# Performance work log

Hardware: AMD Instinct MI355X
Metric: run time of the kernel (lower is better)

Reference implementation:

```python
import jax, jax.numpy as jnp
import numpy as np

B, H, W, C = 16, 64, 64, 192
NH, WS, SHIFT = 6, 8, 4          # heads, window size, shift (window//2)
DEPTH, MLP_R = 2, 4
N = WS * WS                      # tokens per window = 64
HD = C // NH                     # head dim = 32
SCALE = HD ** -0.5
TBL = (2 * WS - 1) ** 2          # relative-bias table size = 225
NW = (H // WS) * (W // WS)       # windows per image = 64


def _rel_pos_index():
    coords = np.stack(np.meshgrid(np.arange(WS), np.arange(WS), indexing='ij')).reshape(2, -1)
    rel = (coords[:, :, None] - coords[:, None, :]).transpose(1, 2, 0)
    rel[..., 0] += WS - 1
    rel[..., 1] += WS - 1
    rel[..., 0] *= 2 * WS - 1
    return jnp.asarray(rel.sum(-1))  # [N, N] int


def _attn_mask():
    # Swin shifted-window mask: region ids then pairwise -100 where ids differ.
    img = np.zeros((H, W))
    sl = (slice(0, -WS), slice(-WS, -SHIFT), slice(-SHIFT, None))
    cnt = 0
    for hs in sl:
        for ws in sl:
            img[hs, ws] = cnt
            cnt += 1
    mw = img.reshape(H // WS, WS, W // WS, WS).transpose(0, 2, 1, 3).reshape(-1, N)
    diff = mw[:, None, :] - mw[:, :, None]
    return jnp.asarray(np.where(diff != 0, -100.0, 0.0).astype(np.float32))  # [NW, N, N]


REL_IDX = _rel_pos_index()
ATTN_MASK = _attn_mask()


def _ln(x, g, b, eps=1e-5):
    mu = x.mean(-1, keepdims=True)
    var = ((x - mu) ** 2).mean(-1, keepdims=True)
    return (x - mu) * jax.lax.rsqrt(var + eps) * g + b


def setup_inputs() -> dict:
    key = jax.random.key(0)
    ks = jax.random.split(key, 8)
    s = 0.02
    return {
        'x': jax.random.normal(ks[0], (B, H * W, C), jnp.float32),
        'norm1_g': jnp.ones((DEPTH, C)), 'norm1_b': jnp.zeros((DEPTH, C)),
        'qkv_w': jax.random.normal(ks[1], (DEPTH, 3 * C, C)) * s,
        'qkv_b': jnp.zeros((DEPTH, 3 * C)),
        'bias_table': jax.random.normal(ks[2], (DEPTH, TBL, NH)) * s,
        'proj_w': jax.random.normal(ks[3], (DEPTH, C, C)) * s,
        'proj_b': jnp.zeros((DEPTH, C)),
        'norm2_g': jnp.ones((DEPTH, C)), 'norm2_b': jnp.zeros((DEPTH, C)),
        'fc1_w': jax.random.normal(ks[4], (DEPTH, MLP_R * C, C)) * s,
        'fc1_b': jnp.zeros((DEPTH, MLP_R * C)),
        'fc2_w': jax.random.normal(ks[5], (DEPTH, C, MLP_R * C)) * s,
        'fc2_b': jnp.zeros((DEPTH, C)),
    }


def _block(x, shift, n1g, n1b, qw, qb, tbl, pw, pb, n2g, n2b, f1w, f1b, f2w, f2b):
    shortcut = x
    y = _ln(x, n1g, n1b).reshape(B, H, W, C)
    if shift > 0:
        y = jnp.roll(y, (-shift, -shift), axis=(1, 2))
    # window partition -> [B*NW, N, C]
    win = y.reshape(B, H // WS, WS, W // WS, WS, C).transpose(0, 1, 3, 2, 4, 5).reshape(-1, N, C)
    qkv = (win @ qw.T + qb).reshape(-1, N, 3, NH, HD).transpose(2, 0, 3, 1, 4)
    q, k, v = qkv[0] * SCALE, qkv[1], qkv[2]          # each [B*NW, NH, N, HD]
    attn = jnp.einsum('bhnd,bhmd->bhnm', q, k)
    attn = attn + tbl[REL_IDX].transpose(2, 0, 1)[None]  # relative position bias
    if shift > 0:
        attn = (attn.reshape(B, NW, NH, N, N) + ATTN_MASK[None, :, None]).reshape(-1, NH, N, N)
    attn = jax.nn.softmax(attn, axis=-1)
    o = jnp.einsum('bhnm,bhmd->bhnd', attn, v).transpose(0, 2, 1, 3).reshape(-1, N, C)
    o = o @ pw.T + pb
    # window reverse
    y = o.reshape(B, H // WS, W // WS, WS, WS, C).transpose(0, 1, 3, 2, 4, 5).reshape(B, H, W, C)
    if shift > 0:
        y = jnp.roll(y, (shift, shift), axis=(1, 2))
    x = shortcut + y.reshape(B, H * W, C)
    h = _ln(x, n2g, n2b)
    h = jax.nn.gelu(h @ f1w.T + f1b, approximate=False)  # torch nn.GELU = exact erf
    return x + (h @ f2w.T + f2b)


def reference(x, norm1_g, norm1_b, qkv_w, qkv_b, bias_table, proj_w, proj_b,
              norm2_g, norm2_b, fc1_w, fc1_b, fc2_w, fc2_b):
    for i in range(DEPTH):
        shift = 0 if i % 2 == 0 else SHIFT
        x = _block(x, shift, norm1_g[i], norm1_b[i], qkv_w[i], qkv_b[i], bias_table[i],
                   proj_w[i], proj_b[i], norm2_g[i], norm2_b[i],
                   fc1_w[i], fc1_b[i], fc2_w[i], fc2_b[i])
    return x
```

## Files before the change

### kernel.cpp

```cpp
#include <hip/hip_runtime.h>
#include <hip/hip_bf16.h>
#include <math.h>

typedef __hip_bfloat16 bf16;
typedef short bf16x8 __attribute__((ext_vector_type(8)));
typedef short s16x4 __attribute__((ext_vector_type(4)));
typedef float f32x4 __attribute__((ext_vector_type(4)));

#define TOKENS 65536
#define C_ 192

__device__ __forceinline__ float b2f(bf16 v){ return __bfloat162float(v); }
__device__ __forceinline__ bf16 f2b(float v){ return __float2bfloat16(v); }
__device__ __forceinline__ short f2s(float v){
  bf16 b = __float2bfloat16(v);
  union { bf16 b; short s; } u; u.b = b; return u.s;
}

__global__ void detect_k(const unsigned* __restrict__ g, int* __restrict__ flag){
  *flag = (g[0] == 0x3F800000u) ? 1 : 0;
}
__global__ void xconv_k(const void* __restrict__ x, float* __restrict__ y, int n,
                        const int* __restrict__ flag){
  int i = blockIdx.x*blockDim.x + threadIdx.x;
  if (i >= n) return;
  if (*flag) y[i] = ((const float*)x)[i];
  else       y[i] = b2f(((const bf16*)x)[i]);
}
struct WPtrs { const void* p[13]; };
__global__ void wconv_all_k(WPtrs wp, const int* __restrict__ offs, const int* __restrict__ lens,
                            bf16* __restrict__ dst, int total, const int* __restrict__ flag){
  int i = blockIdx.x*blockDim.x + threadIdx.x;
  if (i >= total) return;
  int t = 0;
  while (t < 12 && i >= offs[t+1]) t++;
  int j = i - offs[t];
  if (j >= lens[t]) return;
  if (*flag) dst[i] = f2b(((const float*)wp.p[t])[j]);
  else       dst[i] = ((const bf16*)wp.p[t])[j];
}
__global__ void outconv_k(const float* __restrict__ x, void* __restrict__ y, int n,
                          const int* __restrict__ flag){
  int i = blockIdx.x*blockDim.x + threadIdx.x;
  if (i >= n) return;
  if (*flag) ((float*)y)[i] = x[i];
  else       ((bf16*)y)[i]  = f2b(x[i]);
}

__global__ void bias_setup_k(const bf16* __restrict__ bt, float* __restrict__ biasF){
  int idx = blockIdx.x*blockDim.x + threadIdx.x;
  if (idx >= 2*6*64*64) return;
  int v = idx & 63;
  int lane = (idx >> 6) & 63;
  int rest = idx >> 12;
  int head = rest % 6, dd = rest / 6;
  int jt = v >> 4, it = (v >> 2) & 3, r = v & 3;
  int quad = lane >> 4, lr = lane & 15;
  int j = jt*16 + quad*4 + r;
  int i = it*16 + lr;
  int rel = ((i>>3) - (j>>3) + 7)*15 + ((i&7) - (j&7) + 7);
  biasF[idx] = b2f(bt[(dd*225 + rel)*6 + head]);
}

__global__ __launch_bounds__(384, 1) void attn_fused_k(float* __restrict__ xres,
    const bf16* __restrict__ n1g, const bf16* __restrict__ n1b,
    const bf16* __restrict__ qw, const bf16* __restrict__ qb,
    const bf16* __restrict__ pw, const bf16* __restrict__ pb,
    const float* __restrict__ biasF, int shift)
{
  extern __shared__ char smem[];
  short* xo = (short*)smem;
  int win = blockIdx.x;
  int tid = threadIdx.x;
  int wave = tid >> 6, lane = tid & 63;
  int quad = lane >> 4, lr = lane & 15;
  int b_ = win >> 6, wl = win & 63, wh = wl >> 3, wwi = wl & 7;
  short* kh  = (short*)(smem + 25600 + wave*17408);
  short* vth = kh + 2048;
  short* qP  = vth + 2304;

  int c0 = lane*3;
  float g0 = b2f(n1g[c0]), g1 = b2f(n1g[c0+1]), g2 = b2f(n1g[c0+2]);
  float e0 = b2f(n1b[c0]), e1 = b2f(n1b[c0+1]), e2 = b2f(n1b[c0+2]);
  for (int p = 0; p < 11; p++){
    int tok = p*6 + wave;
    if (tok < 64){
      int hh = (wh*8 + (tok>>3) + shift) & 63, ww = (wwi*8 + (tok&7) + shift) & 63;
      const float* rowp = xres + ((size_t)(b_<<12) + (hh<<6) + ww)*C_;
      float v0 = rowp[c0], v1 = rowp[c0+1], v2 = rowp[c0+2];
      float s = v0+v1+v2;
      #pragma unroll
      for (int off=32; off; off>>=1) s += __shfl_xor(s, off);
      float mu = s * (1.0f/192.0f);
      float d0=v0-mu, d1=v1-mu, d2=v2-mu;
      float q = d0*d0+d1*d1+d2*d2;
      #pragma unroll
      for (int off=32; off; off>>=1) q += __shfl_xor(q, off);
      float rstd = rsqrtf(q*(1.0f/192.0f) + 1e-5f);
      xo[tok*200 + c0]   = f2s(d0*rstd*g0 + e0);
      xo[tok*200 + c0+1] = f2s(d1*rstd*g1 + e1);
      xo[tok*200 + c0+2] = f2s(d2*rstd*g2 + e2);
    }
  }
  __syncthreads();

  int head = wave;
  const short* qwd = (const short*)qw;
  #pragma unroll
  for (int cc = 0; cc < 3; cc++){
    int nbase = cc*192 + head*32;
    f32x4 acc[2][4];
    #pragma unroll
    for (int mt = 0; mt < 2; mt++)
      #pragma unroll
      for (int nt = 0; nt < 4; nt++) acc[mt][nt] = (f32x4){0.f,0.f,0.f,0.f};
    #pragma unroll
    for (int ks = 0; ks < 6; ks++){
      bf16x8 af[2], bx[4];
      #pragma unroll
      for (int mt = 0; mt < 2; mt++)
        af[mt] = *(const bf16x8*)(qwd + (size_t)(nbase + mt*16 + lr)*192 + ks*32 + quad*8);
      #pragma unroll
      for (int nt = 0; nt < 4; nt++)
        bx[nt] = *(const bf16x8*)&xo[(nt*16 + lr)*200 + ks*32 + quad*8];
      #pragma unroll
      for (int mt = 0; mt < 2; mt++)
        #pragma unroll
        for (int nt = 0; nt < 4; nt++)
          acc[mt][nt] = __builtin_amdgcn_mfma_f32_16x16x32_bf16(af[mt], bx[nt], acc[mt][nt], 0, 0, 0);
    }
    #pragma unroll
    for (int mt = 0; mt < 2; mt++){
      float bv[4];
      #pragma unroll
      for (int r = 0; r < 4; r++) bv[r] = b2f(qb[nbase + mt*16 + quad*4 + r]);
      #pragma unroll
      for (int nt = 0; nt < 4; nt++){
        int tok = nt*16 + lr;
        if (cc == 0){
          s16x4 pk;
          #pragma unroll
          for (int r = 0; r < 4; r++) pk[r] = f2s((acc[mt][nt][r] + bv[r]) * 0.17677669529663689f);
          *(s16x4*)&qP[tok*32 + mt*16 + quad*4] = pk;
        } else if (cc == 1){
          s16x4 pk;
          #pragma unroll
          for (int r = 0; r < 4; r++) pk[r] = f2s(acc[mt][nt][r] + bv[r]);
          *(s16x4*)&kh[tok*32 + mt*16 + quad*4] = pk;
        } else {
          #pragma unroll
          for (int r = 0; r < 4; r++)
            vth[(mt*16 + quad*4 + r)*72 + tok] = f2s(acc[mt][nt][r] + bv[r]);
        }
      }
    }
  }
  __syncthreads();

  bf16x8 ak[4], bq[4];
  #pragma unroll
  for (int jt = 0; jt < 4; jt++) ak[jt] = *(const bf16x8*)&kh[(jt*16 + lr)*32 + quad*8];
  #pragma unroll
  for (int it = 0; it < 4; it++) bq[it] = *(const bf16x8*)&qP[(it*16 + lr)*32 + quad*8];

  f32x4 S[4][4];
  #pragma unroll
  for (int jt = 0; jt < 4; jt++)
    #pragma unroll
    for (int it = 0; it < 4; it++) S[jt][it] = (f32x4){0.f,0.f,0.f,0.f};
  #pragma unroll
  for (int jt = 0; jt < 4; jt++)
    #pragma unroll
    for (int it = 0; it < 4; it++)
      S[jt][it] = __builtin_amdgcn_mfma_f32_16x16x32_bf16(ak[jt], bq[it], S[jt][it], 0, 0, 0);

  const f32x4* bm = (const f32x4*)(biasF + ((size_t)head*64 + lane)*64);
  #pragma unroll
  for (int jt = 0; jt < 4; jt++)
    #pragma unroll
    for (int it = 0; it < 4; it++) S[jt][it] += bm[jt*4 + it];

  if (shift){
    int idi[4];
    #pragma unroll
    for (int it = 0; it < 4; it++){
      int hh = wh*8 + it*2 + (lr >> 3);
      int wwc = wwi*8 + (lr & 7);
      idi[it] = (hh < 56 ? 0 : (hh < 60 ? 1 : 2))*3 + (wwc < 56 ? 0 : (wwc < 60 ? 1 : 2));
    }
    #pragma unroll
    for (int jt = 0; jt < 4; jt++)
      #pragma unroll
      for (int r = 0; r < 4; r++){
        int j = jt*16 + quad*4 + r;
        int hh = wh*8 + (j >> 3), wwc = wwi*8 + (j & 7);
        int idj = (hh < 56 ? 0 : (hh < 60 ? 1 : 2))*3 + (wwc < 56 ? 0 : (wwc < 60 ? 1 : 2));
        #pragma unroll
        for (int it = 0; it < 4; it++)
          if (idj != idi[it]) S[jt][it][r] -= 100.f;
      }
  }
  #pragma unroll
  for (int it = 0; it < 4; it++){
    float m = -1e30f;
    #pragma unroll
    for (int jt = 0; jt < 4; jt++)
      #pragma unroll
      for (int r = 0; r < 4; r++) m = fmaxf(m, S[jt][it][r]);
    m = fmaxf(m, __shfl_xor(m, 16));
    m = fmaxf(m, __shfl_xor(m, 32));
    float s = 0.f;
    #pragma unroll
    for (int jt = 0; jt < 4; jt++)
      #pragma unroll
      for (int r = 0; r < 4; r++){
        float e = __expf(S[jt][it][r] - m);
        S[jt][it][r] = e; s += e;
      }
    s += __shfl_xor(s, 16);
    s += __shfl_xor(s, 32);
    float inv = 1.0f / s;
    #pragma unroll
    for (int jt = 0; jt < 4; jt++){
      s16x4 pk;
      #pragma unroll
      for (int r = 0; r < 4; r++) pk[r] = f2s(S[jt][it][r] * inv);
      *(s16x4*)&qP[(it*16 + lr)*68 + jt*16 + quad*4] = pk;
    }
  }

  bf16x8 va[2][2], pv[4][2];
  #pragma unroll
  for (int mt = 0; mt < 2; mt++)
    #pragma unroll
    for (int ks = 0; ks < 2; ks++)
      va[mt][ks] = *(const bf16x8*)&vth[(mt*16 + lr)*72 + ks*32 + quad*8];
  #pragma unroll
  for (int nt = 0; nt < 4; nt++)
    #pragma unroll
    for (int ks = 0; ks < 2; ks++)
      pv[nt][ks] = *(const bf16x8*)&qP[(nt*16 + lr)*68 + ks*32 + quad*8];

  f32x4 O[2][4];
  #pragma unroll
  for (int mt = 0; mt < 2; mt++)
    #pragma unroll
    for (int nt = 0; nt < 4; nt++) O[mt][nt] = (f32x4){0.f,0.f,0.f,0.f};
  #pragma unroll
  for (int mt = 0; mt < 2; mt++)
    #pragma unroll
    for (int nt = 0; nt < 4; nt++)
      #pragma unroll
      for (int ks = 0; ks < 2; ks++)
        O[mt][nt] = __builtin_amdgcn_mfma_f32_16x16x32_bf16(va[mt][ks], pv[nt][ks], O[mt][nt], 0, 0, 0);

  #pragma unroll
  for (int mt = 0; mt < 2; mt++)
    #pragma unroll
    for (int nt = 0; nt < 4; nt++){
      s16x4 pk;
      #pragma unroll
      for (int r = 0; r < 4; r++) pk[r] = f2s(O[mt][nt][r]);
      *(s16x4*)&xo[(nt*16 + lr)*200 + head*32 + mt*16 + quad*4] = pk;
    }
  __syncthreads();

  f32x4 po[4][2];
  #pragma unroll
  for (int mt = 0; mt < 4; mt++)
    #pragma unroll
    for (int nt = 0; nt < 2; nt++) po[mt][nt] = (f32x4){0.f,0.f,0.f,0.f};
  const short* pwd = (const short*)pw;
  #pragma unroll
  for (int ks = 0; ks < 6; ks++){
    bf16x8 ao[4], bw[2];
    #pragma unroll
    for (int mt = 0; mt < 4; mt++)
      ao[mt] = *(const bf16x8*)&xo[(mt*16 + lr)*200 + ks*32 + quad*8];
    #pragma unroll
    for (int nt = 0; nt < 2; nt++)
      bw[nt] = *(const bf16x8*)(pwd + (size_t)(head*32 + nt*16 + lr)*192 + ks*32 + quad*8);
    #pragma unroll
    for (int mt = 0; mt < 4; mt++)
      #pragma unroll
      for (int nt = 0; nt < 2; nt++)
        po[mt][nt] = __builtin_amdgcn_mfma_f32_16x16x32_bf16(ao[mt], bw[nt], po[mt][nt], 0, 0, 0);
  }
  #pragma unroll
  for (int nt = 0; nt < 2; nt++){
    int n = head*32 + nt*16 + lr;
    float bv = b2f(pb[n]);
    #pragma unroll
    for (int mt = 0; mt < 4; mt++){
      #pragma unroll
      for (int r = 0; r < 4; r++){
        int tok = mt*16 + quad*4 + r;
        int hh = (wh*8 + (tok>>3) + shift) & 63, ww = (wwi*8 + (tok&7) + shift) & 63;
        float* dst = xres + ((size_t)(b_<<12) + (hh<<6) + ww)*C_ + n;
        *dst += po[mt][nt][r] + bv;
      }
    }
  }
}

__global__ __launch_bounds__(384, 2) void mlp_fused_k(float* __restrict__ xres,
    const bf16* __restrict__ n2g, const bf16* __restrict__ n2b,
    const bf16* __restrict__ f1w, const bf16* __restrict__ f1b,
    const bf16* __restrict__ f2w, const bf16* __restrict__ f2bv)
{
  extern __shared__ char smem[];
  short* xh = (short*)smem;
  short* Hs = (short*)(smem + 51200);
  int t0 = blockIdx.x * 128;
  int tid = threadIdx.x;
  int wave = tid >> 6, lane = tid & 63;
  int quad = lane >> 4, lr = lane & 15;
  int wm = wave / 3, wn = wave % 3;

  int c0 = lane*3;
  float g0 = b2f(n2g[c0]), g1 = b2f(n2g[c0+1]), g2 = b2f(n2g[c0+2]);
  float e0 = b2f(n2b[c0]), e1 = b2f(n2b[c0+1]), e2 = b2f(n2b[c0+2]);
  for (int p = 0; p < 22; p++){
    int row = p*6 + wave;
    if (row < 128){
      const float* rowp = xres + (size_t)(t0 + row)*C_;
      float v0 = rowp[c0], v1 = rowp[c0+1], v2 = rowp[c0+2];
      float s = v0+v1+v2;
      #pragma unroll
      for (int off=32; off; off>>=1) s += __shfl_xor(s, off);
      float mu = s * (1.0f/192.0f);
      float d0=v0-mu, d1=v1-mu, d2=v2-mu;
      float q = d0*d0+d1*d1+d2*d2;
      #pragma unroll
      for (int off=32; off; off>>=1) q += __shfl_xor(q, off);
      float rstd = rsqrtf(q*(1.0f/192.0f) + 1e-5f);
      xh[row*200 + c0]   = f2s(d0*rstd*g0 + e0);
      xh[row*200 + c0+1] = f2s(d1*rstd*g1 + e1);
      xh[row*200 + c0+2] = f2s(d2*rstd*g2 + e2);
    }
  }
  __syncthreads();

  f32x4 acc2[4][4];
  #pragma unroll
  for (int i = 0; i < 4; i++)
    #pragma unroll
    for (int j = 0; j < 4; j++) acc2[i][j] = (f32x4){0.f,0.f,0.f,0.f};

  const short* f1 = (const short*)f1w;
  const short* f2 = (const short*)f2w;
  for (int cc = 0; cc < 8; cc++){
    int hb = cc*96;
    int h0 = hb + wave*16;
    f32x4 a1[8];
    #pragma unroll
    for (int nt = 0; nt < 8; nt++) a1[nt] = (f32x4){0.f,0.f,0.f,0.f};
    #pragma unroll
    for (int ks = 0; ks < 6; ks++){
      bf16x8 af = *(const bf16x8*)(f1 + (size_t)(h0 + lr)*192 + ks*32 + quad*8);
      #pragma unroll
      for (int nt = 0; nt < 8; nt++){
        bf16x8 bx = *(const bf16x8*)&xh[(nt*16 + lr)*200 + ks*32 + quad*8];
        a1[nt] = __builtin_amdgcn_mfma_f32_16x16x32_bf16(af, bx, a1[nt], 0, 0, 0);
      }
    }
    float bv1[4];
    #pragma unroll
    for (int r = 0; r < 4; r++) bv1[r] = b2f(f1b[h0 + quad*4 + r]);
    #pragma unroll
    for (int nt = 0; nt < 8; nt++){
      s16x4 pk;
      #pragma unroll
      for (int r = 0; r < 4; r++){
        float v = a1[nt][r] + bv1[r];
        v = 0.5f*v*(1.0f + erff(v*0.7071067811865476f));
        pk[r] = f2s(v);
      }
      *(s16x4*)&Hs[(nt*16 + lr)*104 + wave*16 + quad*4] = pk;
    }
    __syncthreads();
    #pragma unroll
    for (int ks = 0; ks < 3; ks++){
      bf16x8 ah[4], bw2[4];
      #pragma unroll
      for (int mt = 0; mt < 4; mt++)
        ah[mt] = *(const bf16x8*)&Hs[(wm*64 + mt*16 + lr)*104 + ks*32 + quad*8];
      #pragma unroll
      for (int nt = 0; nt < 4; nt++)
        bw2[nt] = *(const bf16x8*)(f2 + (size_t)(wn*64 + nt*16 + lr)*768 + hb + ks*32 + quad*8);
      #pragma unroll
      for (int mt = 0; mt < 4; mt++)
        #pragma unroll
        for (int nt = 0; nt < 4; nt++)
          acc2[mt][nt] = __builtin_amdgcn_mfma_f32_16x16x32_bf16(ah[mt], bw2[nt], acc2[mt][nt], 0, 0, 0);
    }
    __syncthreads();
  }
  #pragma unroll
  for (int nt = 0; nt < 4; nt++){
    int n = wn*64 + nt*16 + lr;
    float bv = b2f(f2bv[n]);
    #pragma unroll
    for (int mt = 0; mt < 4; mt++){
      #pragma unroll
      for (int r = 0; r < 4; r++){
        int m = wm*64 + mt*16 + quad*4 + r;
        xres[(size_t)(t0 + m)*C_ + n] += acc2[mt][nt][r] + bv;
      }
    }
  }
}

extern "C" void kernel_launch(void* const* d_in, const int* in_sizes, int n_in,
                              void* d_out, int out_size, void* d_ws, size_t ws_size,
                              hipStream_t stream)
{
  (void)in_sizes; (void)n_in; (void)out_size;

  if (ws_size < (size_t)52117000) return;
  char* ws = (char*)d_ws;
  float* xf   = (float*)ws;
  bf16* canon = (bf16*)(ws + 50331648);
  int*  flagp = (int*)(ws + 52116608);
  float* biasF = (float*)d_out;

  static const int W_OFF[13] = {0, 384, 768, 221952, 223104, 225856, 299584,
                                299968, 300352, 300736, 595648, 597184, 892096};
  const int W_TOTAL = 892480;

  hipFuncSetAttribute((const void*)attn_fused_k,
                      hipFuncAttributeMaxDynamicSharedMemorySize, 130048);
  hipFuncSetAttribute((const void*)mlp_fused_k,
                      hipFuncAttributeMaxDynamicSharedMemorySize, 77824);

  detect_k<<<1, 1, 0, stream>>>((const unsigned*)d_in[1], flagp);

  WPtrs wp;
  for (int i = 0; i < 13; i++) wp.p[i] = d_in[i+1];
  {
    int* meta = (int*)(ws + 52116672);
    struct Init {
      static __global__ void run(int* meta){
        const int offs[13] = {0, 384, 768, 221952, 223104, 225856, 299584,
                              299968, 300352, 300736, 595648, 597184, 892096};
        const int lens[13] = {384, 384, 221184, 1152, 2700, 73728, 384,
                              384, 384, 294912, 1536, 294912, 384};
        int i = threadIdx.x;
        if (i < 13){ meta[i] = offs[i]; meta[13+i] = lens[i]; }
      }
    };
    hipLaunchKernelGGL(Init::run, dim3(1), dim3(16), 0, stream, meta);
    wconv_all_k<<<(W_TOTAL + 255)/256, 256, 0, stream>>>(wp, meta, meta+13, canon, W_TOTAL, flagp);
  }

  const int nelem = TOKENS*C_;
  xconv_k<<<nelem/256, 256, 0, stream>>>(d_in[0], xf, nelem, flagp);

  const bf16* n1g = canon + W_OFF[0];
  const bf16* n1b = canon + W_OFF[1];
  const bf16* qw  = canon + W_OFF[2];
  const bf16* qb  = canon + W_OFF[3];
  const bf16* bt  = canon + W_OFF[4];
  const bf16* pw  = canon + W_OFF[5];
  const bf16* pb  = canon + W_OFF[6];
  const bf16* n2g = canon + W_OFF[7];
  const bf16* n2b = canon + W_OFF[8];
  const bf16* f1w = canon + W_OFF[9];
  const bf16* f1b = canon + W_OFF[10];
  const bf16* f2w = canon + W_OFF[11];
  const bf16* f2bv= canon + W_OFF[12];

  bias_setup_k<<<(2*6*64*64)/256, 256, 0, stream>>>(bt, biasF);

  for (int d = 0; d < 2; d++){
    int shift = d ? 4 : 0;
    attn_fused_k<<<1024, 384, 130048, stream>>>(xf,
        n1g + d*192, n1b + d*192, qw + d*576*192, qb + d*576,
        pw + d*192*192, pb + d*192, biasF + d*6*64*64, shift);
    mlp_fused_k<<<512, 384, 77824, stream>>>(xf,
        n2g + d*192, n2b + d*192, f1w + d*768*192, f1b + d*768,
        f2w + d*192*768, f2bv + d*192);
  }
  outconv_k<<<nelem/256, 256, 0, stream>>>(xf, d_out, nelem, flagp);
}
```

Baseline: 663.7 us.

## Split attention heads across two waves and halve MLP token tile

The attention kernel now runs 768 threads per window, with two waves per head each handling half of the query tokens. The projection GEMM is re-tiled across 12 waves, and extra barriers are added so the shared per-head Q/P buffer is not overwritten while the sibling wave still reads it. The MLP kernel now processes 64 tokens per block instead of 128, using half the shared memory, with launch bounds raised to 4 blocks per CU and twice as many blocks. This trades more weight reloads per token and more barriers for higher occupancy and latency hiding.

```diff
diff --git a/kernel.cpp b/kernel.cpp
--- a/kernel.cpp
+++ b/kernel.cpp
@@ -62,7 +62,7 @@
   biasF[idx] = b2f(bt[(dd*225 + rel)*6 + head]);
 }
 
-__global__ __launch_bounds__(384, 1) void attn_fused_k(float* __restrict__ xres,
+__global__ __launch_bounds__(768, 1) void attn_fused_k(float* __restrict__ xres,
     const bf16* __restrict__ n1g, const bf16* __restrict__ n1b,
     const bf16* __restrict__ qw, const bf16* __restrict__ qb,
     const bf16* __restrict__ pw, const bf16* __restrict__ pb,
@@ -74,16 +74,18 @@
   int tid = threadIdx.x;
   int wave = tid >> 6, lane = tid & 63;
   int quad = lane >> 4, lr = lane & 15;
+  int head = wave >> 1, half = wave & 1;
   int b_ = win >> 6, wl = win & 63, wh = wl >> 3, wwi = wl & 7;
-  short* kh  = (short*)(smem + 25600 + wave*17408);
+  short* kh  = (short*)(smem + 25600 + head*17408);
   short* vth = kh + 2048;
   short* qP  = vth + 2304;
 
   int c0 = lane*3;
   float g0 = b2f(n1g[c0]), g1 = b2f(n1g[c0+1]), g2 = b2f(n1g[c0+2]);
   float e0 = b2f(n1b[c0]), e1 = b2f(n1b[c0+1]), e2 = b2f(n1b[c0+2]);
-  for (int p = 0; p < 11; p++){
-    int tok = p*6 + wave;
+  #pragma unroll
+  for (int p = 0; p < 6; p++){
+    int tok = p*12 + wave;
     if (tok < 64){
       int hh = (wh*8 + (tok>>3) + shift) & 63, ww = (wwi*8 + (tok&7) + shift) & 63;
       const float* rowp = xres + ((size_t)(b_<<12) + (hh<<6) + ww)*C_;
@@ -104,29 +106,28 @@
   }
   __syncthreads();
 
-  int head = wave;
   const short* qwd = (const short*)qw;
   #pragma unroll
   for (int cc = 0; cc < 3; cc++){
     int nbase = cc*192 + head*32;
-    f32x4 acc[2][4];
+    f32x4 acc[2][2];
     #pragma unroll
     for (int mt = 0; mt < 2; mt++)
       #pragma unroll
-      for (int nt = 0; nt < 4; nt++) acc[mt][nt] = (f32x4){0.f,0.f,0.f,0.f};
+      for (int nt = 0; nt < 2; nt++) acc[mt][nt] = (f32x4){0.f,0.f,0.f,0.f};
     #pragma unroll
     for (int ks = 0; ks < 6; ks++){
-      bf16x8 af[2], bx[4];
+      bf16x8 af[2], bx[2];
       #pragma unroll
       for (int mt = 0; mt < 2; mt++)
         af[mt] = *(const bf16x8*)(qwd + (size_t)(nbase + mt*16 + lr)*192 + ks*32 + quad*8);
       #pragma unroll
-      for (int nt = 0; nt < 4; nt++)
-        bx[nt] = *(const bf16x8*)&xo[(nt*16 + lr)*200 + ks*32 + quad*8];
+      for (int nt = 0; nt < 2; nt++)
+        bx[nt] = *(const bf16x8*)&xo[((2*half + nt)*16 + lr)*200 + ks*32 + quad*8];
       #pragma unroll
       for (int mt = 0; mt < 2; mt++)
         #pragma unroll
-        for (int nt = 0; nt < 4; nt++)
+        for (int nt = 0; nt < 2; nt++)
           acc[mt][nt] = __builtin_amdgcn_mfma_f32_16x16x32_bf16(af[mt], bx[nt], acc[mt][nt], 0, 0, 0);
     }
     #pragma unroll
@@ -135,8 +136,8 @@
       #pragma unroll
       for (int r = 0; r < 4; r++) bv[r] = b2f(qb[nbase + mt*16 + quad*4 + r]);
       #pragma unroll
-      for (int nt = 0; nt < 4; nt++){
-        int tok = nt*16 + lr;
+      for (int nt = 0; nt < 2; nt++){
+        int tok = (2*half + nt)*16 + lr;
         if (cc == 0){
           s16x4 pk;
           #pragma unroll
@@ -157,34 +158,37 @@
   }
   __syncthreads();
 
-  bf16x8 ak[4], bq[4];
+  bf16x8 ak[4], bq[2];
   #pragma unroll
   for (int jt = 0; jt < 4; jt++) ak[jt] = *(const bf16x8*)&kh[(jt*16 + lr)*32 + quad*8];
   #pragma unroll
-  for (int it = 0; it < 4; it++) bq[it] = *(const bf16x8*)&qP[(it*16 + lr)*32 + quad*8];
-
-  f32x4 S[4][4];
+  for (int it = 0; it < 2; it++)
+    bq[it] = *(const bf16x8*)&qP[((2*half + it)*16 + lr)*32 + quad*8];
+  __syncthreads();
+
+  f32x4 S[4][2];
   #pragma unroll
   for (int jt = 0; jt < 4; jt++)
     #pragma unroll
-    for (int it = 0; it < 4; it++) S[jt][it] = (f32x4){0.f,0.f,0.f,0.f};
+    for (int it = 0; it < 2; it++) S[jt][it] = (f32x4){0.f,0.f,0.f,0.f};
   #pragma unroll
   for (int jt = 0; jt < 4; jt++)
     #pragma unroll
-    for (int it = 0; it < 4; it++)
+    for (int it = 0; it < 2; it++)
       S[jt][it] = __builtin_amdgcn_mfma_f32_16x16x32_bf16(ak[jt], bq[it], S[jt][it], 0, 0, 0);
 
   const f32x4* bm = (const f32x4*)(biasF + ((size_t)head*64 + lane)*64);
   #pragma unroll
   for (int jt = 0; jt < 4; jt++)
     #pragma unroll
-    for (int it = 0; it < 4; it++) S[jt][it] += bm[jt*4 + it];
+    for (int it = 0; it < 2; it++) S[jt][it] += bm[jt*4 + 2*half + it];
 
   if (shift){
-    int idi[4];
-    #pragma unroll
-    for (int it = 0; it < 4; it++){
-      int hh = wh*8 + it*2 + (lr >> 3);
+    int idi[2];
+    #pragma unroll
+    for (int it = 0; it < 2; it++){
+      int itg = 2*half + it;
+      int hh = wh*8 + itg*2 + (lr >> 3);
       int wwc = wwi*8 + (lr & 7);
       idi[it] = (hh < 56 ? 0 : (hh < 60 ? 1 : 2))*3 + (wwc < 56 ? 0 : (wwc < 60 ? 1 : 2));
     }
@@ -196,12 +200,12 @@
         int hh = wh*8 + (j >> 3), wwc = wwi*8 + (j & 7);
         int idj = (hh < 56 ? 0 : (hh < 60 ? 1 : 2))*3 + (wwc < 56 ? 0 : (wwc < 60 ? 1 : 2));
         #pragma unroll
-        for (int it = 0; it < 4; it++)
+        for (int it = 0; it < 2; it++)
           if (idj != idi[it]) S[jt][it][r] -= 100.f;
       }
   }
   #pragma unroll
-  for (int it = 0; it < 4; it++){
+  for (int it = 0; it < 2; it++){
     float m = -1e30f;
     #pragma unroll
     for (int jt = 0; jt < 4; jt++)
@@ -225,31 +229,32 @@
       s16x4 pk;
       #pragma unroll
       for (int r = 0; r < 4; r++) pk[r] = f2s(S[jt][it][r] * inv);
-      *(s16x4*)&qP[(it*16 + lr)*68 + jt*16 + quad*4] = pk;
-    }
-  }
-
-  bf16x8 va[2][2], pv[4][2];
+      *(s16x4*)&qP[((2*half + it)*16 + lr)*68 + jt*16 + quad*4] = pk;
+    }
+  }
+  __syncthreads();
+
+  bf16x8 va[2][2], pv[2][2];
   #pragma unroll
   for (int mt = 0; mt < 2; mt++)
     #pragma unroll
     for (int ks = 0; ks < 2; ks++)
       va[mt][ks] = *(const bf16x8*)&vth[(mt*16 + lr)*72 + ks*32 + quad*8];
   #pragma unroll
-  for (int nt = 0; nt < 4; nt++)
+  for (int nt = 0; nt < 2; nt++)
     #pragma unroll
     for (int ks = 0; ks < 2; ks++)
-      pv[nt][ks] = *(const bf16x8*)&qP[(nt*16 + lr)*68 + ks*32 + quad*8];
-
-  f32x4 O[2][4];
+      pv[nt][ks] = *(const bf16x8*)&qP[((2*half + nt)*16 + lr)*68 + ks*32 + quad*8];
+
+  f32x4 O[2][2];
   #pragma unroll
   for (int mt = 0; mt < 2; mt++)
     #pragma unroll
-    for (int nt = 0; nt < 4; nt++) O[mt][nt] = (f32x4){0.f,0.f,0.f,0.f};
+    for (int nt = 0; nt < 2; nt++) O[mt][nt] = (f32x4){0.f,0.f,0.f,0.f};
   #pragma unroll
   for (int mt = 0; mt < 2; mt++)
     #pragma unroll
-    for (int nt = 0; nt < 4; nt++)
+    for (int nt = 0; nt < 2; nt++)
       #pragma unroll
       for (int ks = 0; ks < 2; ks++)
         O[mt][nt] = __builtin_amdgcn_mfma_f32_16x16x32_bf16(va[mt][ks], pv[nt][ks], O[mt][nt], 0, 0, 0);
@@ -257,44 +262,45 @@
   #pragma unroll
   for (int mt = 0; mt < 2; mt++)
     #pragma unroll
-    for (int nt = 0; nt < 4; nt++){
+    for (int nt = 0; nt < 2; nt++){
       s16x4 pk;
       #pragma unroll
       for (int r = 0; r < 4; r++) pk[r] = f2s(O[mt][nt][r]);
-      *(s16x4*)&xo[(nt*16 + lr)*200 + head*32 + mt*16 + quad*4] = pk;
-    }
-  __syncthreads();
-
-  f32x4 po[4][2];
-  #pragma unroll
-  for (int mt = 0; mt < 4; mt++)
+      *(s16x4*)&xo[((2*half + nt)*16 + lr)*200 + head*32 + mt*16 + quad*4] = pk;
+    }
+  __syncthreads();
+
+  int wm = wave / 6, wn = wave % 6;
+  f32x4 po[2][2];
+  #pragma unroll
+  for (int mt = 0; mt < 2; mt++)
     #pragma unroll
     for (int nt = 0; nt < 2; nt++) po[mt][nt] = (f32x4){0.f,0.f,0.f,0.f};
   const short* pwd = (const short*)pw;
   #pragma unroll
   for (int ks = 0; ks < 6; ks++){
-    bf16x8 ao[4], bw[2];
-    #pragma unroll
-    for (int mt = 0; mt < 4; mt++)
-      ao[mt] = *(const bf16x8*)&xo[(mt*16 + lr)*200 + ks*32 + quad*8];
+    bf16x8 ao[2], bw[2];
+    #pragma unroll
+    for (int mt = 0; mt < 2; mt++)
+      ao[mt] = *(const bf16x8*)&xo[(wm*32 + mt*16 + lr)*200 + ks*32 + quad*8];
     #pragma unroll
     for (int nt = 0; nt < 2; nt++)
-      bw[nt] = *(const bf16x8*)(pwd + (size_t)(head*32 + nt*16 + lr)*192 + ks*32 + quad*8);
-    #pragma unroll
-    for (int mt = 0; mt < 4; mt++)
+      bw[nt] = *(const bf16x8*)(pwd + (size_t)(wn*32 + nt*16 + lr)*192 + ks*32 + quad*8);
+    #pragma unroll
+    for (int mt = 0; mt < 2; mt++)
       #pragma unroll
       for (int nt = 0; nt < 2; nt++)
         po[mt][nt] = __builtin_amdgcn_mfma_f32_16x16x32_bf16(ao[mt], bw[nt], po[mt][nt], 0, 0, 0);
   }
   #pragma unroll
   for (int nt = 0; nt < 2; nt++){
-    int n = head*32 + nt*16 + lr;
+    int n = wn*32 + nt*16 + lr;
     float bv = b2f(pb[n]);
     #pragma unroll
-    for (int mt = 0; mt < 4; mt++){
+    for (int mt = 0; mt < 2; mt++){
       #pragma unroll
       for (int r = 0; r < 4; r++){
-        int tok = mt*16 + quad*4 + r;
+        int tok = wm*32 + mt*16 + quad*4 + r;
         int hh = (wh*8 + (tok>>3) + shift) & 63, ww = (wwi*8 + (tok&7) + shift) & 63;
         float* dst = xres + ((size_t)(b_<<12) + (hh<<6) + ww)*C_ + n;
         *dst += po[mt][nt][r] + bv;
@@ -303,15 +309,15 @@
   }
 }
 
-__global__ __launch_bounds__(384, 2) void mlp_fused_k(float* __restrict__ xres,
+__global__ __launch_bounds__(384, 4) void mlp_fused_k(float* __restrict__ xres,
     const bf16* __restrict__ n2g, const bf16* __restrict__ n2b,
     const bf16* __restrict__ f1w, const bf16* __restrict__ f1b,
     const bf16* __restrict__ f2w, const bf16* __restrict__ f2bv)
 {
   extern __shared__ char smem[];
   short* xh = (short*)smem;
-  short* Hs = (short*)(smem + 51200);
-  int t0 = blockIdx.x * 128;
+  short* Hs = (short*)(smem + 25600);
+  int t0 = blockIdx.x * 64;
   int tid = threadIdx.x;
   int wave = tid >> 6, lane = tid & 63;
   int quad = lane >> 4, lr = lane & 15;
@@ -320,9 +326,10 @@
   int c0 = lane*3;
   float g0 = b2f(n2g[c0]), g1 = b2f(n2g[c0+1]), g2 = b2f(n2g[c0+2]);
   float e0 = b2f(n2b[c0]), e1 = b2f(n2b[c0+1]), e2 = b2f(n2b[c0+2]);
-  for (int p = 0; p < 22; p++){
+  #pragma unroll
+  for (int p = 0; p < 11; p++){
     int row = p*6 + wave;
-    if (row < 128){
+    if (row < 64){
       const float* rowp = xres + (size_t)(t0 + row)*C_;
       float v0 = rowp[c0], v1 = rowp[c0+1], v2 = rowp[c0+2];
       float s = v0+v1+v2;
@@ -341,9 +348,9 @@
   }
   __syncthreads();
 
-  f32x4 acc2[4][4];
-  #pragma unroll
-  for (int i = 0; i < 4; i++)
+  f32x4 acc2[2][4];
+  #pragma unroll
+  for (int i = 0; i < 2; i++)
     #pragma unroll
     for (int j = 0; j < 4; j++) acc2[i][j] = (f32x4){0.f,0.f,0.f,0.f};
 
@@ -352,14 +359,14 @@
   for (int cc = 0; cc < 8; cc++){
     int hb = cc*96;
     int h0 = hb + wave*16;
-    f32x4 a1[8];
-    #pragma unroll
-    for (int nt = 0; nt < 8; nt++) a1[nt] = (f32x4){0.f,0.f,0.f,0.f};
+    f32x4 a1[4];
+    #pragma unroll
+    for (int nt = 0; nt < 4; nt++) a1[nt] = (f32x4){0.f,0.f,0.f,0.f};
     #pragma unroll
     for (int ks = 0; ks < 6; ks++){
       bf16x8 af = *(const bf16x8*)(f1 + (size_t)(h0 + lr)*192 + ks*32 + quad*8);
       #pragma unroll
-      for (int nt = 0; nt < 8; nt++){
+      for (int nt = 0; nt < 4; nt++){
         bf16x8 bx = *(const bf16x8*)&xh[(nt*16 + lr)*200 + ks*32 + quad*8];
         a1[nt] = __builtin_amdgcn_mfma_f32_16x16x32_bf16(af, bx, a1[nt], 0, 0, 0);
       }
@@ -368,7 +375,7 @@
     #pragma unroll
     for (int r = 0; r < 4; r++) bv1[r] = b2f(f1b[h0 + quad*4 + r]);
     #pragma unroll
-    for (int nt = 0; nt < 8; nt++){
+    for (int nt = 0; nt < 4; nt++){
       s16x4 pk;
       #pragma unroll
       for (int r = 0; r < 4; r++){
@@ -376,20 +383,20 @@
         v = 0.5f*v*(1.0f + erff(v*0.7071067811865476f));
         pk[r] = f2s(v);
       }
-      *(s16x4*)&Hs[(nt*16 + lr)*104 + wave*16 + quad*4] = pk;
+      *(s16x4*)&Hs[(nt*16 + lr)*96 + wave*16 + quad*4] = pk;
     }
     __syncthreads();
     #pragma unroll
     for (int ks = 0; ks < 3; ks++){
-      bf16x8 ah[4], bw2[4];
-      #pragma unroll
-      for (int mt = 0; mt < 4; mt++)
-        ah[mt] = *(const bf16x8*)&Hs[(wm*64 + mt*16 + lr)*104 + ks*32 + quad*8];
+      bf16x8 ah[2], bw2[4];
+      #pragma unroll
+      for (int mt = 0; mt < 2; mt++)
+        ah[mt] = *(const bf16x8*)&Hs[(wm*32 + mt*16 + lr)*96 + ks*32 + quad*8];
       #pragma unroll
       for (int nt = 0; nt < 4; nt++)
         bw2[nt] = *(const bf16x8*)(f2 + (size_t)(wn*64 + nt*16 + lr)*768 + hb + ks*32 + quad*8);
       #pragma unroll
-      for (int mt = 0; mt < 4; mt++)
+      for (int mt = 0; mt < 2; mt++)
         #pragma unroll
         for (int nt = 0; nt < 4; nt++)
           acc2[mt][nt] = __builtin_amdgcn_mfma_f32_16x16x32_bf16(ah[mt], bw2[nt], acc2[mt][nt], 0, 0, 0);
@@ -401,10 +408,10 @@
     int n = wn*64 + nt*16 + lr;
     float bv = b2f(f2bv[n]);
     #pragma unroll
-    for (int mt = 0; mt < 4; mt++){
+    for (int mt = 0; mt < 2; mt++){
       #pragma unroll
       for (int r = 0; r < 4; r++){
-        int m = wm*64 + mt*16 + quad*4 + r;
+        int m = wm*32 + mt*16 + quad*4 + r;
         xres[(size_t)(t0 + m)*C_ + n] += acc2[mt][nt][r] + bv;
       }
     }
@@ -431,7 +438,7 @@
   hipFuncSetAttribute((const void*)attn_fused_k,
                       hipFuncAttributeMaxDynamicSharedMemorySize, 130048);
   hipFuncSetAttribute((const void*)mlp_fused_k,
-                      hipFuncAttributeMaxDynamicSharedMemorySize, 77824);
+                      hipFuncAttributeMaxDynamicSharedMemorySize, 37888);
 
   detect_k<<<1, 1, 0, stream>>>((const unsigned*)d_in[1], flagp);
 
@@ -474,10 +481,10 @@
 
   for (int d = 0; d < 2; d++){
     int shift = d ? 4 : 0;
-    attn_fused_k<<<1024, 384, 130048, stream>>>(xf,
+    attn_fused_k<<<1024, 768, 130048, stream>>>(xf,
         n1g + d*192, n1b + d*192, qw + d*576*192, qb + d*576,
         pw + d*192*192, pb + d*192, biasF + d*6*64*64, shift);
-    mlp_fused_k<<<512, 384, 77824, stream>>>(xf,
+    mlp_fused_k<<<1024, 384, 37888, stream>>>(xf,
         n2g + d*192, n2b + d*192, f1w + d*768*192, f1b + d*768,
         f2w + d*192*768, f2bv + d*192);
   }
```

New measurement: 694.2 us. +4.6%, slower.
